# Kernel tuning notes

Measured on AMD Instinct MI355X. Metric: run time of the kernel, lower is better.

## Reference

```python
import jax, jax.numpy as jnp
from jax import lax
import numpy as np

B, H, W = 64, 256, 256          # batch, image height/width
CH = 16                          # channel (first conv out)
NCLS = 8                         # len(ansmap) + 1
HID = 128                        # LSTM hidden
ARR = 256                        # arr_size (flattened conv output = LSTM seq len)


def setup_inputs() -> dict:
    key = jax.random.key(0)
    ks = jax.random.split(key, 24)
    n = lambda k, s: jax.random.normal(k, s, dtype=jnp.float32)
    inp = {
        "x": n(ks[0], (B, 3, H, W)),
        # conv stage 1: Conv2d(3, CH, 2, 2) + BatchNorm2d(CH) (eval-mode stats)
        "conv1_w": n(ks[1], (CH, 3, 2, 2)) * 0.2,
        "conv1_b": n(ks[2], (CH,)) * 0.1,
        "bn1_g": jnp.ones((CH,), jnp.float32),
        "bn1_b": jnp.zeros((CH,), jnp.float32),
        "bn1_m": n(ks[3], (CH,)) * 0.1,
        "bn1_v": jax.random.uniform(ks[4], (CH,), jnp.float32, 0.5, 1.5),
        # conv stage 2: Conv2d(CH, 1, 2, 2) + BatchNorm2d(1)
        "conv2_w": n(ks[5], (1, CH, 2, 2)) * 0.2,
        "conv2_b": n(ks[6], (1,)) * 0.1,
        "bn2_g": jnp.ones((1,), jnp.float32),
        "bn2_b": jnp.zeros((1,), jnp.float32),
        "bn2_m": n(ks[7], (1,)) * 0.1,
        "bn2_v": jax.random.uniform(ks[8], (1,), jnp.float32, 0.5, 1.5),
        # prestack MLP: Linear(256,32) -> ReLU -> Linear(32,32) -> ReLU -> Linear(32,8) -> Softmax
        "pre_w1": n(ks[9], (32, ARR)) * 0.05,
        "pre_b1": n(ks[10], (32,)) * 0.05,
        "pre_w2": n(ks[11], (32, 32)) * 0.1,
        "pre_b2": n(ks[12], (32,)) * 0.05,
        "pre_w3": n(ks[13], (NCLS, 32)) * 0.1,
        "pre_b3": n(ks[14], (NCLS,)) * 0.05,
        # per-class LSTMs: LSTM(1, HID, batch_first=True), torch gate order i,f,g,o
        "lstm_wih": n(ks[15], (NCLS, 4 * HID, 1)) * 0.1,
        "lstm_whh": n(ks[16], (NCLS, 4 * HID, HID)) * 0.05,
        "lstm_bih": n(ks[17], (NCLS, 4 * HID)) * 0.05,
        "lstm_bhh": n(ks[18], (NCLS, 4 * HID)) * 0.05,
        # per-class persistent hidden state parameters hn[i]: (1, B, HID)
        "hn": n(ks[19], (NCLS, 1, B, HID)) * 0.1,
        # final stack: Linear(256, 8) after AvgPool2d((NCLS,1)) + Flatten
        "out_w": n(ks[20], (NCLS, ARR)) * 0.05,
        "out_b": n(ks[21], (NCLS,)) * 0.05,
    }
    return inp


def reference(x, conv1_w, conv1_b, bn1_g, bn1_b, bn1_m, bn1_v,
              conv2_w, conv2_b, bn2_g, bn2_b, bn2_m, bn2_v,
              pre_w1, pre_b1, pre_w2, pre_b2, pre_w3, pre_b3,
              lstm_wih, lstm_whh, lstm_bih, lstm_bhh, hn, out_w, out_b):
    def conv(z, w, b, s):
        y = lax.conv_general_dilated(z, w, (s, s), 'VALID',
                                     dimension_numbers=('NCHW', 'OIHW', 'NCHW'))
        return y + b[None, :, None, None]

    def bn(z, g, b, m, v):
        scale = g / jnp.sqrt(v + 1e-5)
        return (z - m[None, :, None, None]) * scale[None, :, None, None] + b[None, :, None, None]

    def maxpool2(z):
        return lax.reduce_window(z, -jnp.inf, lax.max, (1, 1, 2, 2), (1, 1, 2, 2), 'VALID')

    # conv feature extractor (the python map over x is just the batch dim)
    c = maxpool2(jax.nn.relu(bn(conv(x, conv1_w, conv1_b, 2), bn1_g, bn1_b, bn1_m, bn1_v)))
    c = maxpool2(jax.nn.relu(bn(conv(c, conv2_w, conv2_b, 2), bn2_g, bn2_b, bn2_m, bn2_v)))
    c = c.reshape(B, ARR)  # Flatten(0) per sample -> [B, 256]

    # prestack MLP + softmax over classes, then torch-style reshape (NCLS, B, 1)
    h1 = jax.nn.relu(c @ pre_w1.T + pre_b1)
    h2 = jax.nn.relu(h1 @ pre_w2.T + pre_b2)
    pre = jax.nn.softmax(h2 @ pre_w3.T + pre_b3, axis=1)  # [B, NCLS]
    pre = pre.reshape(NCLS, B, 1)  # row-major reshape, as in torch .reshape

    seq = c.reshape(B, ARR, 1)  # LSTM input, shared across all classes

    def lstm_last_unit(wih, whh, bih, bhh, h0):
        # wih [4H,1], whh [4H,H], h0 [B,H]; returns o[:, :, -1] -> [B, T]
        xg = jnp.einsum('bti,gi->btg', seq, wih) + bih  # precomputed input gates [B,T,4H]

        def step(carry, xgt):
            h, cc = carry
            gates = xgt + h @ whh.T + bhh  # [B, 4H]
            i, f, g, o = jnp.split(gates, 4, axis=-1)
            cc = jax.nn.sigmoid(f) * cc + jax.nn.sigmoid(i) * jnp.tanh(g)
            h = jax.nn.sigmoid(o) * jnp.tanh(cc)
            return (h, cc), h[:, -1]  # only last hidden feature is consumed

        (_, _), last = lax.scan(step, (h0, jnp.zeros_like(h0)), jnp.swapaxes(xg, 0, 1))
        return jnp.swapaxes(last, 0, 1)  # [B, T]

    h0 = hn[:, 0]  # [NCLS, B, HID]
    o_last = jax.vmap(lstm_last_unit)(lstm_wih, lstm_whh, lstm_bih, lstm_bhh, h0)  # [NCLS,B,T]

    r = (o_last * pre).transpose(1, 0, 2)  # [B, NCLS, T]
    avg = r.mean(axis=1)                   # AvgPool2d((NCLS,1)) + Flatten -> [B, T]
    return avg @ out_w.T + out_b           # [B, NCLS]
```

## Files before the change

kernel.cpp:

```cpp
#include <hip/hip_runtime.h>
#include <hip/hip_bf16.h>
#include <hip/hip_fp16.h>


typedef _Float16 h2_t __attribute__((ext_vector_type(2)));
typedef unsigned int u32x4 __attribute__((ext_vector_type(4)));

__device__ __forceinline__ float dot2f(unsigned int w, unsigned int h, float acc) {
    return __builtin_amdgcn_fdot2(__builtin_bit_cast(h2_t, w),
                                  __builtin_bit_cast(h2_t, h), acc, false);
}
__device__ __forceinline__ float sigmoidf_(float x) {
    return 1.0f / (1.0f + __expf(-x));
}
__device__ __forceinline__ float tanhf_(float x) {
    float t = __expf(-2.0f * fabsf(x));
    float r = (1.0f - t) / (1.0f + t);
    return copysignf(r, x);
}
__device__ __forceinline__ unsigned short f2h(float x) {
    __half h = __float2half(x);
    return *(unsigned short*)&h;
}

__global__ __launch_bounds__(256) void k_cvt(
    const float* __restrict__ w, unsigned int* __restrict__ wh)
{
    int i = blockIdx.x * 256 + threadIdx.x;
    float2 f = ((const float2*)w)[i];
    unsigned short lo = f2h(f.x), hi = f2h(f.y);
    wh[i] = ((unsigned int)hi << 16) | lo;
}

__global__ __launch_bounds__(256) void k_conv1(
    const float* __restrict__ x, const float* __restrict__ w,
    const float* __restrict__ cb, const float* __restrict__ g,
    const float* __restrict__ bb, const float* __restrict__ m,
    const float* __restrict__ v, float* __restrict__ c1)
{
    __shared__ __align__(16) float w1s[192];
    __shared__ float As[16], Cs[16];
    int tid = threadIdx.x;
    if (tid < 192) w1s[tid] = w[tid];
    if (tid < 16) {
        float s = g[tid] / sqrtf(v[tid] + 1e-5f);
        As[tid] = s;
        Cs[tid] = (cb[tid] - m[tid]) * s + bb[tid];
    }
    __syncthreads();

    int gid = blockIdx.x * 256 + tid;
    int b   = gid >> 12;
    int rem = gid & 4095;
    int oi  = rem >> 6, oj = rem & 63;

    float xr[3][4][4];
    #pragma unroll
    for (int ci = 0; ci < 3; ++ci) {
        #pragma unroll
        for (int r = 0; r < 4; ++r) {
            const float4 t4 = *(const float4*)(x +
                (((size_t)(b * 3 + ci) * 256 + (4 * oi + r)) * 256 + 4 * oj));
            xr[ci][r][0] = t4.x; xr[ci][r][1] = t4.y;
            xr[ci][r][2] = t4.z; xr[ci][r][3] = t4.w;
        }
    }
    const float4* w4 = (const float4*)w1s;
    #pragma unroll
    for (int co = 0; co < 16; ++co) {
        float val[2][2] = {{0.f, 0.f}, {0.f, 0.f}};
        #pragma unroll
        for (int ci = 0; ci < 3; ++ci) {
            float4 wq = w4[co * 3 + ci];
            #pragma unroll
            for (int pi = 0; pi < 2; ++pi) {
                #pragma unroll
                for (int pj = 0; pj < 2; ++pj) {
                    float a = val[pi][pj];
                    a = fmaf(xr[ci][2*pi  ][2*pj  ], wq.x, a);
                    a = fmaf(xr[ci][2*pi  ][2*pj+1], wq.y, a);
                    a = fmaf(xr[ci][2*pi+1][2*pj  ], wq.z, a);
                    a = fmaf(xr[ci][2*pi+1][2*pj+1], wq.w, a);
                    val[pi][pj] = a;
                }
            }
        }
        float A = As[co], C = Cs[co];
        float mx = 0.0f;
        #pragma unroll
        for (int pi = 0; pi < 2; ++pi)
            #pragma unroll
            for (int pj = 0; pj < 2; ++pj)
                mx = fmaxf(mx, fmaf(A, val[pi][pj], C));
        c1[((size_t)(b * 16 + co) * 64 + oi) * 64 + oj] = mx;
    }
}

__global__ __launch_bounds__(256) void k_conv2(
    const float* __restrict__ c1, const float* __restrict__ w2,
    const float* __restrict__ cb, const float* __restrict__ g,
    const float* __restrict__ bb, const float* __restrict__ m,
    const float* __restrict__ v, float* __restrict__ c)
{
    __shared__ float w2s[64];
    int tid = threadIdx.x;
    if (tid < 64) w2s[tid] = w2[tid];
    __syncthreads();
    float A2 = g[0] / sqrtf(v[0] + 1e-5f);
    float C2 = (cb[0] - m[0]) * A2 + bb[0];

    int gid = blockIdx.x * 256 + tid;
    int b   = gid >> 8;
    int rem = gid & 255;
    int oi  = rem >> 4, oj = rem & 15;

    float val[2][2] = {{0.f, 0.f}, {0.f, 0.f}};
    for (int ci = 0; ci < 16; ++ci) {
        float xr[4][4];
        #pragma unroll
        for (int r = 0; r < 4; ++r) {
            float4 t4 = *(const float4*)(c1 +
                (((size_t)(b * 16 + ci) * 64 + (4 * oi + r)) * 64 + 4 * oj));
            xr[r][0] = t4.x; xr[r][1] = t4.y; xr[r][2] = t4.z; xr[r][3] = t4.w;
        }
        float w0 = w2s[ci*4+0], w1 = w2s[ci*4+1], w2v = w2s[ci*4+2], w3 = w2s[ci*4+3];
        #pragma unroll
        for (int pi = 0; pi < 2; ++pi) {
            #pragma unroll
            for (int pj = 0; pj < 2; ++pj) {
                float a = val[pi][pj];
                a = fmaf(xr[2*pi  ][2*pj  ], w0, a);
                a = fmaf(xr[2*pi  ][2*pj+1], w1, a);
                a = fmaf(xr[2*pi+1][2*pj  ], w2v, a);
                a = fmaf(xr[2*pi+1][2*pj+1], w3, a);
                val[pi][pj] = a;
            }
        }
    }
    float mx = 0.0f;
    #pragma unroll
    for (int pi = 0; pi < 2; ++pi)
        #pragma unroll
        for (int pj = 0; pj < 2; ++pj)
            mx = fmaxf(mx, fmaf(A2, val[pi][pj], C2));
    c[(size_t)b * 256 + oi * 16 + oj] = mx;
}

__global__ __launch_bounds__(64) void k_mlp(
    const float* __restrict__ c,
    const float* __restrict__ w1, const float* __restrict__ b1,
    const float* __restrict__ w2, const float* __restrict__ b2,
    const float* __restrict__ w3, const float* __restrict__ b3,
    float* __restrict__ S)
{
    __shared__ __align__(16) float cs[256];
    __shared__ float h1s[32], h2s[32], ls[8];
    int b = blockIdx.x, tid = threadIdx.x;
    *(float4*)&cs[tid * 4] = *(const float4*)(c + (size_t)b * 256 + tid * 4);
    __syncthreads();
    if (tid < 32) {
        float acc = b1[tid];
        for (int k = 0; k < 256; ++k) acc = fmaf(cs[k], w1[tid * 256 + k], acc);
        h1s[tid] = fmaxf(acc, 0.f);
    }
    __syncthreads();
    if (tid < 32) {
        float acc = b2[tid];
        #pragma unroll
        for (int k = 0; k < 32; ++k) acc = fmaf(h1s[k], w2[tid * 32 + k], acc);
        h2s[tid] = fmaxf(acc, 0.f);
    }
    __syncthreads();
    if (tid < 8) {
        float acc = b3[tid];
        #pragma unroll
        for (int k = 0; k < 32; ++k) acc = fmaf(h2s[k], w3[tid * 32 + k], acc);
        ls[tid] = acc;
    }
    __syncthreads();
    if (tid == 0) {
        float mx = ls[0];
        #pragma unroll
        for (int k = 1; k < 8; ++k) mx = fmaxf(mx, ls[k]);
        float e[8]; float sum = 0.f;
        #pragma unroll
        for (int k = 0; k < 8; ++k) { e[k] = expf(ls[k] - mx); sum += e[k]; }
        float inv = 1.0f / sum;
        #pragma unroll
        for (int k = 0; k < 8; ++k) S[b * 8 + k] = e[k] * inv;
    }
}

__global__
__attribute__((amdgpu_flat_work_group_size(512, 512), amdgpu_waves_per_eu(1, 2)))
void k_lstm(
    const unsigned int* __restrict__ whh_h, const float* __restrict__ wih,
    const float* __restrict__ bih, const float* __restrict__ bhh,
    const float* __restrict__ hn,  const float* __restrict__ c,
    float* __restrict__ lasth)
{
    __shared__ __align__(16) unsigned short h_h[2][128];
    __shared__ float g_lds[2][512];
    __shared__ __align__(16) float c_lds[2][256];

    int tid   = threadIdx.x;
    int kcls  = blockIdx.x >> 5;
    int bbase = (blockIdx.x & 31) * 2;

    const u32x4* wp = (const u32x4*)(whh_h + ((size_t)(kcls * 512 + tid)) * 64);
    u32x4 u0  = wp[0],  u1  = wp[1],  u2  = wp[2],  u3  = wp[3];
    u32x4 u4  = wp[4],  u5  = wp[5],  u6  = wp[6],  u7  = wp[7];
    u32x4 u8  = wp[8],  u9  = wp[9],  u10 = wp[10], u11 = wp[11];
    u32x4 u12 = wp[12], u13 = wp[13], u14 = wp[14], u15 = wp[15];
    asm volatile("" : "+v"(u0), "+v"(u1), "+v"(u2),  "+v"(u3),
                      "+v"(u4), "+v"(u5), "+v"(u6),  "+v"(u7));
    asm volatile("" : "+v"(u8), "+v"(u9), "+v"(u10), "+v"(u11),
                      "+v"(u12),"+v"(u13),"+v"(u14), "+v"(u15));

    float xw   = wih[kcls * 512 + tid];
    float bias = bih[kcls * 512 + tid] + bhh[kcls * 512 + tid];
    int gtype  = tid >> 7;

    if (tid < 256) {
        int b = tid >> 7, j = tid & 127;
        h_h[b][j] = f2h(hn[((size_t)kcls * 64 + bbase + b) * 128 + j]);
    }
    if (tid < 128) {
        int f = tid * 4; int b = f >> 8; int off = f & 255;
        *(float4*)&c_lds[b][off] = *(const float4*)(c + (size_t)(bbase + b) * 256 + off);
    }
    float cc = 0.0f;
    __syncthreads();

    const u32x4* hq0 = (const u32x4*)&h_h[0][0];
    const u32x4* hq1 = (const u32x4*)&h_h[1][0];

#define DSTEP(I, A0, A1, B0, B1)                                        \
    {                                                                   \
        u32x4 q0 = hq0[I]; u32x4 q1 = hq1[I];                           \
        A0 = dot2f(u##I[0], q0[0], A0); A1 = dot2f(u##I[0], q1[0], A1); \
        B0 = dot2f(u##I[1], q0[1], B0); B1 = dot2f(u##I[1], q1[1], B1); \
        A0 = dot2f(u##I[2], q0[2], A0); A1 = dot2f(u##I[2], q1[2], A1); \
        B0 = dot2f(u##I[3], q0[3], B0); B1 = dot2f(u##I[3], q1[3], B1); \
    }

    for (int t = 0; t < 256; ++t) {
        float a0 = fmaf(c_lds[0][t], xw, bias);
        float a1 = fmaf(c_lds[1][t], xw, bias);
        float b0 = 0.0f, b1 = 0.0f;
        DSTEP(0,  a0, a1, b0, b1) DSTEP(1,  a0, a1, b0, b1)
        DSTEP(2,  a0, a1, b0, b1) DSTEP(3,  a0, a1, b0, b1)
        DSTEP(4,  a0, a1, b0, b1) DSTEP(5,  a0, a1, b0, b1)
        DSTEP(6,  a0, a1, b0, b1) DSTEP(7,  a0, a1, b0, b1)
        DSTEP(8,  a0, a1, b0, b1) DSTEP(9,  a0, a1, b0, b1)
        DSTEP(10, a0, a1, b0, b1) DSTEP(11, a0, a1, b0, b1)
        DSTEP(12, a0, a1, b0, b1) DSTEP(13, a0, a1, b0, b1)
        DSTEP(14, a0, a1, b0, b1) DSTEP(15, a0, a1, b0, b1)
        float v0 = a0 + b0, v1 = a1 + b1;
        if (gtype == 2) { v0 = tanhf_(v0);    v1 = tanhf_(v1);    }
        else            { v0 = sigmoidf_(v0); v1 = sigmoidf_(v1); }
        g_lds[0][tid] = v0;
        g_lds[1][tid] = v1;
        __syncthreads();

        if (tid < 256) {
            int b = tid >> 7, j = tid & 127;
            float gi = g_lds[b][j];
            float gf = g_lds[b][128 + j];
            float gg = g_lds[b][256 + j];
            float go = g_lds[b][384 + j];
            cc = gf * cc + gi * gg;
            float h = go * tanhf_(cc);
            h_h[b][j] = f2h(h);
            if (j == 127)
                lasth[((size_t)kcls * 64 + bbase + b) * 256 + t] = h;
        }
        __syncthreads();
    }
#undef DSTEP
}

__global__ __launch_bounds__(256) void k_out(
    const float* __restrict__ lasth, const float* __restrict__ S,
    const float* __restrict__ out_w, const float* __restrict__ out_b,
    float* __restrict__ out)
{
    __shared__ __align__(16) float avg[256];
    int b = blockIdx.x, t = threadIdx.x;
    float a = 0.f;
    #pragma unroll
    for (int k = 0; k < 8; ++k) {
        a = fmaf(S[k * 64 + b], lasth[((size_t)k * 64 + b) * 256 + t], a);
    }
    avg[t] = a * 0.125f;
    __syncthreads();
    if (t < 8) {
        float acc = out_b[t];
        for (int tt = 0; tt < 256; ++tt)
            acc = fmaf(avg[tt], out_w[t * 256 + tt], acc);
        out[b * 8 + t] = acc;
    }
}

extern "C" void kernel_launch(void* const* d_in, const int* in_sizes, int n_in,
                              void* d_out, int out_size, void* d_ws, size_t ws_size,
                              hipStream_t stream) {
    const float* x       = (const float*)d_in[0];
    const float* conv1_w = (const float*)d_in[1];
    const float* conv1_b = (const float*)d_in[2];
    const float* bn1_g   = (const float*)d_in[3];
    const float* bn1_b   = (const float*)d_in[4];
    const float* bn1_m   = (const float*)d_in[5];
    const float* bn1_v   = (const float*)d_in[6];
    const float* conv2_w = (const float*)d_in[7];
    const float* conv2_b = (const float*)d_in[8];
    const float* bn2_g   = (const float*)d_in[9];
    const float* bn2_b   = (const float*)d_in[10];
    const float* bn2_m   = (const float*)d_in[11];
    const float* bn2_v   = (const float*)d_in[12];
    const float* pre_w1  = (const float*)d_in[13];
    const float* pre_b1  = (const float*)d_in[14];
    const float* pre_w2  = (const float*)d_in[15];
    const float* pre_b2  = (const float*)d_in[16];
    const float* pre_w3  = (const float*)d_in[17];
    const float* pre_b3  = (const float*)d_in[18];
    const float* lstm_wih = (const float*)d_in[19];
    const float* lstm_whh = (const float*)d_in[20];
    const float* lstm_bih = (const float*)d_in[21];
    const float* lstm_bhh = (const float*)d_in[22];
    const float* hn      = (const float*)d_in[23];
    const float* out_w   = (const float*)d_in[24];
    const float* out_b   = (const float*)d_in[25];

    float* ws    = (float*)d_ws;
    float* c1    = ws;
    float* c     = c1 + 4194304;
    float* S     = c + 16384;
    float* lasth = S + 512;
    unsigned int* whh_h = (unsigned int*)c1;

    k_conv1<<<1024, 256, 0, stream>>>(x, conv1_w, conv1_b, bn1_g, bn1_b, bn1_m, bn1_v, c1);
    k_conv2<<<64, 256, 0, stream>>>(c1, conv2_w, conv2_b, bn2_g, bn2_b, bn2_m, bn2_v, c);
    k_mlp<<<64, 64, 0, stream>>>(c, pre_w1, pre_b1, pre_w2, pre_b2, pre_w3, pre_b3, S);
    k_cvt<<<1024, 256, 0, stream>>>(lstm_whh, whh_h);
    k_lstm<<<256, 512, 0, stream>>>(whh_h, lstm_wih, lstm_bih, lstm_bhh, hn, c, lasth);
    k_out<<<64, 256, 0, stream>>>(lasth, S, out_w, out_b, (float*)d_out);
}
```

Baseline: 296.3 us.

## Split each LSTM gate row's recurrent dot product across two lanes

```diff
diff --git a/kernel.cpp b/kernel.cpp
--- a/kernel.cpp
+++ b/kernel.cpp
@@ -192,38 +192,37 @@
 }
 
 __global__
-__attribute__((amdgpu_flat_work_group_size(512, 512), amdgpu_waves_per_eu(1, 2)))
+__attribute__((amdgpu_flat_work_group_size(1024, 1024), amdgpu_waves_per_eu(4, 4)))
 void k_lstm(
     const unsigned int* __restrict__ whh_h, const float* __restrict__ wih,
     const float* __restrict__ bih, const float* __restrict__ bhh,
     const float* __restrict__ hn,  const float* __restrict__ c,
     float* __restrict__ lasth)
 {
-    __shared__ __align__(16) unsigned short h_h[2][128];
+    __shared__ __align__(16) unsigned short h_h[2][136];
     __shared__ float g_lds[2][512];
     __shared__ __align__(16) float c_lds[2][256];
 
     int tid   = threadIdx.x;
+    int g     = tid >> 1;
+    int kh    = tid & 1;
     int kcls  = blockIdx.x >> 5;
     int bbase = (blockIdx.x & 31) * 2;
 
-    const u32x4* wp = (const u32x4*)(whh_h + ((size_t)(kcls * 512 + tid)) * 64);
-    u32x4 u0  = wp[0],  u1  = wp[1],  u2  = wp[2],  u3  = wp[3];
-    u32x4 u4  = wp[4],  u5  = wp[5],  u6  = wp[6],  u7  = wp[7];
-    u32x4 u8  = wp[8],  u9  = wp[9],  u10 = wp[10], u11 = wp[11];
-    u32x4 u12 = wp[12], u13 = wp[13], u14 = wp[14], u15 = wp[15];
-    asm volatile("" : "+v"(u0), "+v"(u1), "+v"(u2),  "+v"(u3),
-                      "+v"(u4), "+v"(u5), "+v"(u6),  "+v"(u7));
-    asm volatile("" : "+v"(u8), "+v"(u9), "+v"(u10), "+v"(u11),
-                      "+v"(u12),"+v"(u13),"+v"(u14), "+v"(u15));
-
-    float xw   = wih[kcls * 512 + tid];
-    float bias = bih[kcls * 512 + tid] + bhh[kcls * 512 + tid];
-    int gtype  = tid >> 7;
+    const u32x4* wp = (const u32x4*)(whh_h + ((size_t)(kcls * 512 + g)) * 64 + kh * 32);
+    u32x4 u0 = wp[0], u1 = wp[1], u2 = wp[2], u3 = wp[3];
+    u32x4 u4 = wp[4], u5 = wp[5], u6 = wp[6], u7 = wp[7];
+    asm volatile("" : "+v"(u0), "+v"(u1), "+v"(u2), "+v"(u3),
+                      "+v"(u4), "+v"(u5), "+v"(u6), "+v"(u7));
+
+    float xw   = wih[kcls * 512 + g];
+    float bias = bih[kcls * 512 + g] + bhh[kcls * 512 + g];
+    int gtype  = g >> 7;
 
     if (tid < 256) {
         int b = tid >> 7, j = tid & 127;
-        h_h[b][j] = f2h(hn[((size_t)kcls * 64 + bbase + b) * 128 + j]);
+        int js = j + ((j >> 6) << 3);
+        h_h[b][js] = f2h(hn[((size_t)kcls * 64 + bbase + b) * 128 + j]);
     }
     if (tid < 128) {
         int f = tid * 4; int b = f >> 8; int off = f & 255;
@@ -232,8 +231,8 @@
     float cc = 0.0f;
     __syncthreads();
 
-    const u32x4* hq0 = (const u32x4*)&h_h[0][0];
-    const u32x4* hq1 = (const u32x4*)&h_h[1][0];
+    const u32x4* hq0 = (const u32x4*)((const unsigned int*)&h_h[0][0] + kh * 36);
+    const u32x4* hq1 = (const u32x4*)((const unsigned int*)&h_h[1][0] + kh * 36);
 
 #define DSTEP(I, A0, A1, B0, B1)                                        \
     {                                                                   \
@@ -245,22 +244,19 @@
     }
 
     for (int t = 0; t < 256; ++t) {
-        float a0 = fmaf(c_lds[0][t], xw, bias);
-        float a1 = fmaf(c_lds[1][t], xw, bias);
+        float a0 = kh ? 0.0f : fmaf(c_lds[0][t], xw, bias);
+        float a1 = kh ? 0.0f : fmaf(c_lds[1][t], xw, bias);
         float b0 = 0.0f, b1 = 0.0f;
-        DSTEP(0,  a0, a1, b0, b1) DSTEP(1,  a0, a1, b0, b1)
-        DSTEP(2,  a0, a1, b0, b1) DSTEP(3,  a0, a1, b0, b1)
-        DSTEP(4,  a0, a1, b0, b1) DSTEP(5,  a0, a1, b0, b1)
-        DSTEP(6,  a0, a1, b0, b1) DSTEP(7,  a0, a1, b0, b1)
-        DSTEP(8,  a0, a1, b0, b1) DSTEP(9,  a0, a1, b0, b1)
-        DSTEP(10, a0, a1, b0, b1) DSTEP(11, a0, a1, b0, b1)
-        DSTEP(12, a0, a1, b0, b1) DSTEP(13, a0, a1, b0, b1)
-        DSTEP(14, a0, a1, b0, b1) DSTEP(15, a0, a1, b0, b1)
-        float v0 = a0 + b0, v1 = a1 + b1;
-        if (gtype == 2) { v0 = tanhf_(v0);    v1 = tanhf_(v1);    }
-        else            { v0 = sigmoidf_(v0); v1 = sigmoidf_(v1); }
-        g_lds[0][tid] = v0;
-        g_lds[1][tid] = v1;
+        DSTEP(0, a0, a1, b0, b1) DSTEP(1, a0, a1, b0, b1)
+        DSTEP(2, a0, a1, b0, b1) DSTEP(3, a0, a1, b0, b1)
+        DSTEP(4, a0, a1, b0, b1) DSTEP(5, a0, a1, b0, b1)
+        DSTEP(6, a0, a1, b0, b1) DSTEP(7, a0, a1, b0, b1)
+        a0 += b0; a1 += b1;
+        a0 += __shfl_xor(a0, 1);
+        a1 += __shfl_xor(a1, 1);
+        float vv = kh ? a1 : a0;
+        vv = (gtype == 2) ? tanhf_(vv) : sigmoidf_(vv);
+        g_lds[kh][g] = vv;
         __syncthreads();
 
         if (tid < 256) {
@@ -271,7 +267,8 @@
             float go = g_lds[b][384 + j];
             cc = gf * cc + gi * gg;
             float h = go * tanhf_(cc);
-            h_h[b][j] = f2h(h);
+            int js = j + ((j >> 6) << 3);
+            h_h[b][js] = f2h(h);
             if (j == 127)
                 lasth[((size_t)kcls * 64 + bbase + b) * 256 + t] = h;
         }
@@ -343,6 +340,6 @@
     k_conv2<<<64, 256, 0, stream>>>(c1, conv2_w, conv2_b, bn2_g, bn2_b, bn2_m, bn2_v, c);
     k_mlp<<<64, 64, 0, stream>>>(c, pre_w1, pre_b1, pre_w2, pre_b2, pre_w3, pre_b3, S);
     k_cvt<<<1024, 256, 0, stream>>>(lstm_whh, whh_h);
-    k_lstm<<<256, 512, 0, stream>>>(whh_h, lstm_wih, lstm_bih, lstm_bhh, hn, c, lasth);
+    k_lstm<<<256, 1024, 0, stream>>>(whh_h, lstm_wih, lstm_bih, lstm_bhh, hn, c, lasth);
     k_out<<<64, 256, 0, stream>>>(lasth, S, out_w, out_b, (float*)d_out);
 }
```

Result: slower. 319.5 us (+7.8%).
